# Performance work log

Measured on AMD Instinct MI355X. Metric: run time of the kernel, lower is better.

## Reference

```python
import jax, jax.numpy as jnp
import numpy as np

N_STEPS = 8  # DGL GatedGraphConv n_steps as hardcoded in GatedGCN.__init__


def _gru(a, h, Wih, Whh, bih, bhh):
    # torch.nn.GRUCell: gate order (r, z, n)
    gi = a @ Wih.T + bih          # [N, 3d]
    gh = h @ Whh.T + bhh          # [N, 3d]
    ir, iz, inn = jnp.split(gi, 3, axis=-1)
    hr, hz, hn = jnp.split(gh, 3, axis=-1)
    r = jax.nn.sigmoid(ir + hr)
    z = jax.nn.sigmoid(iz + hz)
    n = jnp.tanh(inn + r * hn)
    return (1.0 - z) * n + z * h


def _gated_conv(h, src, dst, W, b, Wih, Whh, bih, bhh):
    # DGL GatedGraphConv with a single etype: for each step,
    # message = Linear(h[src]); aggregate = sum over in-edges; h = GRU(agg, h)
    N = h.shape[0]

    def step(h, _):
        m = h @ W.T + b                                   # [N, d] linear per node (message fn)
        agg = jax.ops.segment_sum(m[src], dst, num_segments=N)  # [N, d] sum over in-edges
        return _gru(agg, h, Wih, Whh, bih, bhh), None

    h, _ = jax.lax.scan(step, h, None, length=N_STEPS)
    return h


def setup_inputs() -> dict:
    key = jax.random.key(0)
    ks = jax.random.split(key, 10)
    N, E, D = 50000, 800000, 128  # in_feats = h_feats = num_classes = 128
    s = 1.0 / np.sqrt(D)
    return {
        "in_feat": jax.random.normal(ks[0], (N, D), jnp.float32),
        "src": jax.random.randint(ks[1], (E,), 0, N),
        "dst": jax.random.randint(ks[2], (E,), 0, N),
        "W1": jax.random.normal(ks[3], (D, D), jnp.float32) * s,
        "b1": jnp.zeros((D,), jnp.float32),
        "Wih1": jax.random.normal(ks[4], (3 * D, D), jnp.float32) * s,
        "Whh1": jax.random.normal(ks[5], (3 * D, D), jnp.float32) * s,
        "bih1": jnp.zeros((3 * D,), jnp.float32),
        "bhh1": jnp.zeros((3 * D,), jnp.float32),
        "W2": jax.random.normal(ks[6], (D, D), jnp.float32) * s,
        "b2": jnp.zeros((D,), jnp.float32),
        "Wih2": jax.random.normal(ks[7], (3 * D, D), jnp.float32) * s,
        "Whh2": jax.random.normal(ks[8], (3 * D, D), jnp.float32) * s,
        "bih2": jnp.zeros((3 * D,), jnp.float32),
        "bhh2": jnp.zeros((3 * D,), jnp.float32),
    }


def reference(in_feat, src, dst, W1, b1, Wih1, Whh1, bih1, bhh1,
              W2, b2, Wih2, Whh2, bih2, bhh2):
    # in_feats == h_feats so DGL's zero-padding of the input is a no-op here.
    h = _gated_conv(in_feat, src, dst, W1, b1, Wih1, Whh1, bih1, bhh1)
    h = jax.nn.relu(h)
    h = _gated_conv(h, src, dst, W2, b2, Wih2, Whh2, bih2, bhh2)
    # dgl.mean_nodes with a single graph -> [1, num_classes]
    return jnp.mean(h, axis=0, keepdims=True)
```

## Files before the change

kernel.cpp:

```cpp
#include <hip/hip_runtime.h>
#include <hip/hip_bf16.h>
#include <cmath>

#define DD 128

typedef __attribute__((ext_vector_type(8))) short short8v;
typedef __attribute__((ext_vector_type(4))) short short4v;
typedef __attribute__((ext_vector_type(4))) float floatx4;

__device__ __forceinline__ float sigmoid_f(float x) { return 1.0f / (1.0f + __expf(-x)); }
__device__ __forceinline__ float tanh_f(float x) {
  float e = __expf(2.0f * x);
  return 1.0f - 2.0f / (e + 1.0f);
}
__device__ __forceinline__ unsigned short f2bf(float x) {
  __hip_bfloat16 b = __float2bfloat16(x);
  return *reinterpret_cast<unsigned short*>(&b);
}
__device__ __forceinline__ float bf2f(unsigned short s) {
  return __uint_as_float(((unsigned int)s) << 16);
}

__global__ __launch_bounds__(256) void deg_count(const int* __restrict__ dst,
                                                 int* __restrict__ deg, int E) {
  int e = blockIdx.x * blockDim.x + threadIdx.x;
  if (e < E) atomicAdd(&deg[dst[e]], 1);
}

__global__ __launch_bounds__(256) void scan_part(const int* __restrict__ deg,
                                                 int* __restrict__ bsum, int N) {
  __shared__ int s[256];
  int tid = threadIdx.x;
  int i = blockIdx.x * 256 + tid;
  s[tid] = (i < N) ? deg[i] : 0;
  __syncthreads();
  for (int st = 128; st > 0; st >>= 1) {
    if (tid < st) s[tid] += s[tid + st];
    __syncthreads();
  }
  if (tid == 0) bsum[blockIdx.x] = s[0];
}

__global__ __launch_bounds__(256) void scan_top(const int* __restrict__ bsum,
                                                int* __restrict__ bofs, int nb) {
  __shared__ int s[256];
  int tid = threadIdx.x;
  int v = (tid < nb) ? bsum[tid] : 0;
  s[tid] = v;
  __syncthreads();
  for (int o = 1; o < 256; o <<= 1) {
    int t = (tid >= o) ? s[tid - o] : 0;
    __syncthreads();
    s[tid] += t;
    __syncthreads();
  }
  if (tid < nb) bofs[tid] = s[tid] - v;
  if (tid == nb - 1) bofs[nb] = s[tid];
}

__global__ __launch_bounds__(256) void scan_final(const int* __restrict__ deg,
                                                  const int* __restrict__ bofs,
                                                  int* __restrict__ ofs,
                                                  int* __restrict__ cur, int N) {
  __shared__ int s[256];
  int tid = threadIdx.x;
  int i = blockIdx.x * 256 + tid;
  int v = (i < N) ? deg[i] : 0;
  s[tid] = v;
  __syncthreads();
  for (int o = 1; o < 256; o <<= 1) {
    int t = (tid >= o) ? s[tid - o] : 0;
    __syncthreads();
    s[tid] += t;
    __syncthreads();
  }
  int off = bofs[blockIdx.x] + s[tid] - v;
  if (i < N) {
    ofs[i] = off;
    cur[i] = off;
    if (i == N - 1) ofs[N] = off + v;
  }
}

__global__ __launch_bounds__(256) void fill_csr(const int* __restrict__ src,
                                                const int* __restrict__ dst,
                                                int* __restrict__ cur,
                                                int* __restrict__ eidx, int E) {
  int e = blockIdx.x * blockDim.x + threadIdx.x;
  if (e < E) {
    int p = atomicAdd(&cur[dst[e]], 1);
    eidx[p] = src[e];
  }
}

__global__ __launch_bounds__(128) void fuse_w(const float* __restrict__ Wih,
                                              const float* __restrict__ W,
                                              float* __restrict__ Wc32) {
  int r = blockIdx.x;
  int k = threadIdx.x;
  float acc = 0.0f;
  for (int j = 0; j < DD; ++j) acc = fmaf(Wih[r * DD + j], W[j * DD + k], acc);
  Wc32[(size_t)r * DD + k] = acc;
}

__global__ __launch_bounds__(128) void fuse_u(const float* __restrict__ Wih,
                                              const float* __restrict__ b,
                                              float* __restrict__ u) {
  int r = blockIdx.x * 128 + threadIdx.x;
  if (r < 3 * DD) {
    float acc = 0.0f;
    for (int j = 0; j < DD; ++j) acc = fmaf(Wih[r * DD + j], b[j], acc);
    u[r] = acc;
  }
}

__global__ __launch_bounds__(256) void split_w(const float* __restrict__ Wf,
                                               const float* __restrict__ Whh,
                                               unsigned short* __restrict__ Wp) {
  int i = blockIdx.x * 256 + threadIdx.x;
  const int TOT = 6 * DD * DD;
  if (i < TOT) {
    int r = i >> 7;
    float x = (r < 3 * DD) ? Wf[i] : Whh[i - 3 * DD * DD];
    unsigned short hb = f2bf(x);
    float xr = x - bf2f(hb);
    unsigned short mb = f2bf(xr);
    Wp[i] = hb;
    Wp[TOT + i] = mb;
  }
}

__global__ __launch_bounds__(256) void gather_h(const float* __restrict__ h,
                                                const int* __restrict__ ofs,
                                                const int* __restrict__ eidx,
                                                unsigned short* __restrict__ aggp, int N) {
  int node = blockIdx.x * 8 + (threadIdx.x >> 5);
  if (node >= N) return;
  int l = (threadIdx.x & 31) << 2;
  int beg = ofs[node], end = ofs[node + 1];
  float4 aa[4];
#pragma unroll
  for (int j = 0; j < 4; ++j) aa[j] = (float4){0.f, 0.f, 0.f, 0.f};
  int e = beg;
  for (; e + 7 < end; e += 8) {
    float4 v[8];
#pragma unroll
    for (int j = 0; j < 8; ++j)
      v[j] = *(const float4*)(h + (size_t)eidx[e + j] * DD + l);
#pragma unroll
    for (int j = 0; j < 8; ++j) {
      aa[j & 3].x += v[j].x; aa[j & 3].y += v[j].y;
      aa[j & 3].z += v[j].z; aa[j & 3].w += v[j].w;
    }
  }
  for (; e + 1 < end; e += 2) {
    float4 v0 = *(const float4*)(h + (size_t)eidx[e] * DD + l);
    float4 v1 = *(const float4*)(h + (size_t)eidx[e + 1] * DD + l);
    aa[0].x += v0.x; aa[0].y += v0.y; aa[0].z += v0.z; aa[0].w += v0.w;
    aa[1].x += v1.x; aa[1].y += v1.y; aa[1].z += v1.z; aa[1].w += v1.w;
  }
  if (e < end) {
    float4 v = *(const float4*)(h + (size_t)eidx[e] * DD + l);
    aa[0].x += v.x; aa[0].y += v.y; aa[0].z += v.z; aa[0].w += v.w;
  }
  float f[4];
  f[0] = (aa[0].x + aa[1].x) + (aa[2].x + aa[3].x);
  f[1] = (aa[0].y + aa[1].y) + (aa[2].y + aa[3].y);
  f[2] = (aa[0].z + aa[1].z) + (aa[2].z + aa[3].z);
  f[3] = (aa[0].w + aa[1].w) + (aa[2].w + aa[3].w);
  short4v q0, q1;
#pragma unroll
  for (int j = 0; j < 4; ++j) {
    unsigned short hb = f2bf(f[j]);
    float xr = f[j] - bf2f(hb);
    q0[j] = (short)hb;
    q1[j] = (short)f2bf(xr);
  }
  unsigned short* p = aggp + (size_t)node * 256 + l;
  *(short4v*)(p) = q0;
  *(short4v*)(p + 128) = q1;
}

__device__ __forceinline__ void split8_2v(float4 v0, float4 v1, short8v& q0, short8v& q1) {
  float f[8] = {v0.x, v0.y, v0.z, v0.w, v1.x, v1.y, v1.z, v1.w};
#pragma unroll
  for (int e = 0; e < 8; ++e) {
    float x = f[e];
    unsigned short hb = f2bf(x);
    float xr = x - bf2f(hb);
    q0[e] = (short)hb;
    q1[e] = (short)f2bf(xr);
  }
}

__global__ __launch_bounds__(256, 3) void gru_mfma3(
    const unsigned short* __restrict__ Aggp,
    const float* __restrict__ H,
    const unsigned short* __restrict__ Wp,
    const float* __restrict__ bih, const float* __restrict__ bhh,
    const float* __restrict__ u, const int* __restrict__ deg,
    float* __restrict__ Hout, int N, int do_relu)
{
  __shared__ short sB[2][96 * DD];
  const int TOT = 6 * DD * DD;
  const int tid = threadIdx.x;
  const int wid = tid >> 6;
  const int lane = tid & 63;
  const int lrow = lane & 15;
  const int hi = lane >> 4;
  const int lk = hi * 8;
  const int rowBase = blockIdx.x * 128 + wid * 32;
  const int j0 = blockIdx.y * 32;

  floatx4 acc[6][2][2];
#pragma unroll
  for (int g = 0; g < 6; ++g)
#pragma unroll
    for (int ct = 0; ct < 2; ++ct)
#pragma unroll
      for (int rt = 0; rt < 2; ++rt) acc[g][ct][rt] = (floatx4){0.f, 0.f, 0.f, 0.f};

  int r0 = rowBase + lrow;       if (r0 >= N) r0 = N - 1;
  int r1 = rowBase + 16 + lrow;  if (r1 >= N) r1 = N - 1;

  int s_row[6], s_cnk[6];
  size_t s_grow[6];
#pragma unroll
  for (int i = 0; i < 6; ++i) {
    int ch = tid + i * 256;
    s_row[i] = ch >> 4;
    s_cnk[i] = ch & 15;
    s_grow[i] = (size_t)((s_row[i] >> 5) * DD + j0 + (s_row[i] & 31));
  }

#pragma unroll
  for (int arr = 0; arr < 2; ++arr) {
    const size_t gbase = (size_t)arr * 384 * DD;
    if (arr > 0) __syncthreads();

    {
      short8v w0[6], w1[6];
#pragma unroll
      for (int i = 0; i < 6; ++i) {
        w0[i] = *(const short8v*)(Wp + 0 * TOT + gbase + s_grow[i] * DD + s_cnk[i] * 8);
        w1[i] = *(const short8v*)(Wp + 1 * TOT + gbase + s_grow[i] * DD + s_cnk[i] * 8);
      }
#pragma unroll
      for (int i = 0; i < 6; ++i) {
        int off = s_row[i] * DD + (s_cnk[i] ^ (s_row[i] & 7)) * 8;
        *(short8v*)(&sB[0][off]) = w0[i];
        *(short8v*)(&sB[1][off]) = w1[i];
      }
    }
    __syncthreads();

    if (arr == 0) {
      const unsigned short* P0 = Aggp + (size_t)r0 * 256 + lk;
      const unsigned short* P1 = Aggp + (size_t)r1 * 256 + lk;
      __builtin_amdgcn_s_setprio(1);
#pragma unroll
      for (int kc = 0; kc < 4; ++kc) {
        short8v f00 = *(const short8v*)(P0 + kc * 32);
        short8v f10 = *(const short8v*)(P0 + 128 + kc * 32);
        short8v f01 = *(const short8v*)(P1 + kc * 32);
        short8v f11 = *(const short8v*)(P1 + 128 + kc * 32);
#pragma unroll
        for (int gl = 0; gl < 3; ++gl) {
#pragma unroll
          for (int ct = 0; ct < 2; ++ct) {
            int lr = gl * 32 + ct * 16 + lrow;
            int off = lr * DD + ((kc * 4 + hi) ^ (lr & 7)) * 8;
            short8v bh = *(const short8v*)(&sB[0][off]);
            acc[gl][ct][0] = __builtin_amdgcn_mfma_f32_16x16x32_bf16(f00, bh, acc[gl][ct][0], 0, 0, 0);
            acc[gl][ct][0] = __builtin_amdgcn_mfma_f32_16x16x32_bf16(f10, bh, acc[gl][ct][0], 0, 0, 0);
            acc[gl][ct][1] = __builtin_amdgcn_mfma_f32_16x16x32_bf16(f01, bh, acc[gl][ct][1], 0, 0, 0);
            acc[gl][ct][1] = __builtin_amdgcn_mfma_f32_16x16x32_bf16(f11, bh, acc[gl][ct][1], 0, 0, 0);
            short8v bm = *(const short8v*)(&sB[1][off]);
            acc[gl][ct][0] = __builtin_amdgcn_mfma_f32_16x16x32_bf16(f00, bm, acc[gl][ct][0], 0, 0, 0);
            acc[gl][ct][1] = __builtin_amdgcn_mfma_f32_16x16x32_bf16(f01, bm, acc[gl][ct][1], 0, 0, 0);
          }
        }
      }
      __builtin_amdgcn_s_setprio(0);
    } else {
      const float* A0 = H + (size_t)r0 * DD + lk;
      const float* A1 = H + (size_t)r1 * DD + lk;
      float4 pa0 = *(const float4*)(A0);
      float4 pa1 = *(const float4*)(A0 + 4);
      float4 pb0 = *(const float4*)(A1);
      float4 pb1 = *(const float4*)(A1 + 4);

      __builtin_amdgcn_s_setprio(1);
#pragma unroll
      for (int kc = 0; kc < 4; ++kc) {
        float4 qa0, qa1, qb0, qb1;
        if (kc < 3) {
          qa0 = *(const float4*)(A0 + (kc + 1) * 32);
          qa1 = *(const float4*)(A0 + (kc + 1) * 32 + 4);
          qb0 = *(const float4*)(A1 + (kc + 1) * 32);
          qb1 = *(const float4*)(A1 + (kc + 1) * 32 + 4);
        }
        short8v f00, f10, f01, f11;
        split8_2v(pa0, pa1, f00, f10);
        split8_2v(pb0, pb1, f01, f11);
#pragma unroll
        for (int gl = 0; gl < 3; ++gl) {
#pragma unroll
          for (int ct = 0; ct < 2; ++ct) {
            int lr = gl * 32 + ct * 16 + lrow;
            int off = lr * DD + ((kc * 4 + hi) ^ (lr & 7)) * 8;
            short8v bh = *(const short8v*)(&sB[0][off]);
            acc[3 + gl][ct][0] = __builtin_amdgcn_mfma_f32_16x16x32_bf16(f00, bh, acc[3 + gl][ct][0], 0, 0, 0);
            acc[3 + gl][ct][0] = __builtin_amdgcn_mfma_f32_16x16x32_bf16(f10, bh, acc[3 + gl][ct][0], 0, 0, 0);
            acc[3 + gl][ct][1] = __builtin_amdgcn_mfma_f32_16x16x32_bf16(f01, bh, acc[3 + gl][ct][1], 0, 0, 0);
            acc[3 + gl][ct][1] = __builtin_amdgcn_mfma_f32_16x16x32_bf16(f11, bh, acc[3 + gl][ct][1], 0, 0, 0);
            short8v bm = *(const short8v*)(&sB[1][off]);
            acc[3 + gl][ct][0] = __builtin_amdgcn_mfma_f32_16x16x32_bf16(f00, bm, acc[3 + gl][ct][0], 0, 0, 0);
            acc[3 + gl][ct][1] = __builtin_amdgcn_mfma_f32_16x16x32_bf16(f01, bm, acc[3 + gl][ct][1], 0, 0, 0);
          }
        }
        if (kc < 3) { pa0 = qa0; pa1 = qa1; pb0 = qb0; pb1 = qb1; }
      }
      __builtin_amdgcn_s_setprio(0);
    }
  }

  float bi_r[2], bi_z[2], bi_n[2], bh_r[2], bh_z[2], bh_n[2], u_r[2], u_z[2], u_n[2];
#pragma unroll
  for (int ct = 0; ct < 2; ++ct) {
    int c = j0 + ct * 16 + lrow;
    bi_r[ct] = bih[c];  bi_z[ct] = bih[DD + c];  bi_n[ct] = bih[2 * DD + c];
    bh_r[ct] = bhh[c];  bh_z[ct] = bhh[DD + c];  bh_n[ct] = bhh[2 * DD + c];
    u_r[ct]  = u[c];    u_z[ct]  = u[DD + c];    u_n[ct]  = u[2 * DD + c];
  }

#pragma unroll
  for (int rt = 0; rt < 2; ++rt) {
#pragma unroll
    for (int q = 0; q < 4; ++q) {
      int row = rowBase + rt * 16 + hi * 4 + q;
      if (row < N) {
        float dg = (float)deg[row];
#pragma unroll
        for (int ct = 0; ct < 2; ++ct) {
          int c = j0 + ct * 16 + lrow;
          float ir = acc[0][ct][rt][q] + bi_r[ct] + dg * u_r[ct];
          float iz = acc[1][ct][rt][q] + bi_z[ct] + dg * u_z[ct];
          float in = acc[2][ct][rt][q] + bi_n[ct] + dg * u_n[ct];
          float hr = acc[3][ct][rt][q] + bh_r[ct];
          float hz = acc[4][ct][rt][q] + bh_z[ct];
          float hn = acc[5][ct][rt][q] + bh_n[ct];
          float rg = sigmoid_f(ir + hr);
          float zg = sigmoid_f(iz + hz);
          float ng = tanh_f(in + rg * hn);
          float hold = H[(size_t)row * DD + c];
          float out = (1.0f - zg) * ng + zg * hold;
          if (do_relu) out = fmaxf(out, 0.0f);
          Hout[(size_t)row * DD + c] = out;
        }
      }
    }
  }
}

__global__ __launch_bounds__(256) void col_mean(
    const float* __restrict__ H, float* __restrict__ out, int N)
{
  __shared__ float s[256];
  int c = threadIdx.x & 127;
  int rg = threadIdx.x >> 7;
  float acc = 0.0f;
  for (int r = blockIdx.x * 2 + rg; r < N; r += gridDim.x * 2)
    acc += H[(size_t)r * DD + c];
  s[threadIdx.x] = acc;
  __syncthreads();
  if (threadIdx.x < 128) {
    float v = (s[threadIdx.x] + s[threadIdx.x + 128]) * (1.0f / (float)N);
    unsafeAtomicAdd(out + c, v);
  }
}

extern "C" void kernel_launch(void* const* d_in, const int* in_sizes, int n_in,
                              void* d_out, int out_size, void* d_ws, size_t ws_size,
                              hipStream_t stream) {
  const float* in_feat = (const float*)d_in[0];
  const int* src = (const int*)d_in[1];
  const int* dst = (const int*)d_in[2];
  const float* W[2]   = {(const float*)d_in[3], (const float*)d_in[9]};
  const float* bb[2]  = {(const float*)d_in[4], (const float*)d_in[10]};
  const float* Wih[2] = {(const float*)d_in[5], (const float*)d_in[11]};
  const float* Whh[2] = {(const float*)d_in[6], (const float*)d_in[12]};
  const float* bih[2] = {(const float*)d_in[7], (const float*)d_in[13]};
  const float* bhh[2] = {(const float*)d_in[8], (const float*)d_in[14]};
  const int N = in_sizes[0] / DD;
  const int E = in_sizes[1];

  const size_t nd = (size_t)N * DD;
  char* base = (char*)d_ws;
  float* hA  = (float*)base; base += nd * sizeof(float);
  float* hB  = (float*)base; base += nd * sizeof(float);
  unsigned short* aggp = (unsigned short*)base; base += (size_t)N * 256 * sizeof(unsigned short);
  float* Wc32 = (float*)base; base += (size_t)3 * DD * DD * sizeof(float);
  unsigned short* Wp[2];
  Wp[0] = (unsigned short*)base; base += (size_t)2 * 6 * DD * DD * sizeof(unsigned short);
  Wp[1] = (unsigned short*)base; base += (size_t)2 * 6 * DD * DD * sizeof(unsigned short);
  float* u[2];
  u[0] = (float*)base; base += 3 * DD * sizeof(float);
  u[1] = (float*)base; base += 3 * DD * sizeof(float);
  int* deg  = (int*)base; base += (size_t)N * sizeof(int);
  int* ofs  = (int*)base; base += ((size_t)N + 1) * sizeof(int);
  int* cur  = (int*)base; base += (size_t)N * sizeof(int);
  int* eidx = (int*)base; base += (size_t)E * sizeof(int);
  int* bsum = (int*)base; base += 256 * sizeof(int);
  int* bofs = (int*)base; base += 257 * sizeof(int);

  const int nb = (N + 255) / 256;

  hipMemsetAsync(deg, 0, (size_t)N * sizeof(int), stream);
  deg_count<<<(E + 255) / 256, 256, 0, stream>>>(dst, deg, E);
  scan_part<<<nb, 256, 0, stream>>>(deg, bsum, N);
  scan_top<<<1, 256, 0, stream>>>(bsum, bofs, nb);
  scan_final<<<nb, 256, 0, stream>>>(deg, bofs, ofs, cur, N);
  fill_csr<<<(E + 255) / 256, 256, 0, stream>>>(src, dst, cur, eidx, E);

  for (int layer = 0; layer < 2; ++layer) {
    fuse_w<<<3 * DD, 128, 0, stream>>>(Wih[layer], W[layer], Wc32);
    split_w<<<(6 * DD * DD + 255) / 256, 256, 0, stream>>>(Wc32, Whh[layer], Wp[layer]);
    fuse_u<<<3, 128, 0, stream>>>(Wih[layer], bb[layer], u[layer]);
  }

  hipMemcpyAsync(hA, in_feat, nd * sizeof(float), hipMemcpyDeviceToDevice, stream);

  float* hcur = hA;
  float* hnxt = hB;
  const int gblocks = (N + 7) / 8;
  const int mblocks = (N + 127) / 128;

  for (int layer = 0; layer < 2; ++layer) {
    for (int step_i = 0; step_i < 8; ++step_i) {
      gather_h<<<gblocks, 256, 0, stream>>>(hcur, ofs, eidx, aggp, N);
      int do_relu = (layer == 0 && step_i == 7) ? 1 : 0;
      gru_mfma3<<<dim3(mblocks, 4), 256, 0, stream>>>(
          aggp, hcur, Wp[layer], bih[layer], bhh[layer],
          u[layer], deg, hnxt, N, do_relu);
      float* t = hcur; hcur = hnxt; hnxt = t;
    }
  }

  hipMemsetAsync(d_out, 0, DD * sizeof(float), stream);
  col_mean<<<256, 256, 0, stream>>>(hcur, (float*)d_out, N);
}
```

Baseline: 1.813 ms.

## Halve GRU tile rows and single-buffer weight LDS to raise occupancy

The GRU MFMA kernel now gives each wave 16 rows instead of 32 (64 rows per block), roughly doubling the grid. Only one half of the split bf16 weight slab sits in shared memory at a time, loaded in two passes with extra barriers. A-fragments are preloaded before the weight passes, and launch bounds rise to 4 blocks per CU. This cuts LDS and register footprint to raise occupancy, but each block reloads the full weights from global/L2 for half as many rows and synchronises more often.

```diff
diff --git a/kernel.cpp b/kernel.cpp
--- a/kernel.cpp
+++ b/kernel.cpp
@@ -193,7 +193,7 @@
   }
 }
 
-__global__ __launch_bounds__(256, 3) void gru_mfma3(
+__global__ __launch_bounds__(256, 4) void gru_mfma3(
     const unsigned short* __restrict__ Aggp,
     const float* __restrict__ H,
     const unsigned short* __restrict__ Wp,
@@ -201,7 +201,7 @@
     const float* __restrict__ u, const int* __restrict__ deg,
     float* __restrict__ Hout, int N, int do_relu)
 {
-  __shared__ short sB[2][96 * DD];
+  __shared__ short sB[96 * DD];
   const int TOT = 6 * DD * DD;
   const int tid = threadIdx.x;
   const int wid = tid >> 6;
@@ -209,19 +209,17 @@
   const int lrow = lane & 15;
   const int hi = lane >> 4;
   const int lk = hi * 8;
-  const int rowBase = blockIdx.x * 128 + wid * 32;
+  const int rowBase = blockIdx.x * 64 + wid * 16;
   const int j0 = blockIdx.y * 32;
 
-  floatx4 acc[6][2][2];
+  floatx4 acc[6][2];
 #pragma unroll
   for (int g = 0; g < 6; ++g)
 #pragma unroll
-    for (int ct = 0; ct < 2; ++ct)
-#pragma unroll
-      for (int rt = 0; rt < 2; ++rt) acc[g][ct][rt] = (floatx4){0.f, 0.f, 0.f, 0.f};
-
-  int r0 = rowBase + lrow;       if (r0 >= N) r0 = N - 1;
-  int r1 = rowBase + 16 + lrow;  if (r1 >= N) r1 = N - 1;
+    for (int ct = 0; ct < 2; ++ct) acc[g][ct] = (floatx4){0.f, 0.f, 0.f, 0.f};
+
+  int r0 = rowBase + lrow;
+  if (r0 >= N) r0 = N - 1;
 
   int s_row[6], s_cnk[6];
   size_t s_grow[6];
@@ -236,90 +234,57 @@
 #pragma unroll
   for (int arr = 0; arr < 2; ++arr) {
     const size_t gbase = (size_t)arr * 384 * DD;
-    if (arr > 0) __syncthreads();
-
-    {
-      short8v w0[6], w1[6];
-#pragma unroll
-      for (int i = 0; i < 6; ++i) {
-        w0[i] = *(const short8v*)(Wp + 0 * TOT + gbase + s_grow[i] * DD + s_cnk[i] * 8);
-        w1[i] = *(const short8v*)(Wp + 1 * TOT + gbase + s_grow[i] * DD + s_cnk[i] * 8);
+
+    short8v frag0[4], frag1[4];
+    if (arr == 0) {
+      const unsigned short* P0 = Aggp + (size_t)r0 * 256 + lk;
+#pragma unroll
+      for (int kc = 0; kc < 4; ++kc) {
+        frag0[kc] = *(const short8v*)(P0 + kc * 32);
+        frag1[kc] = *(const short8v*)(P0 + 128 + kc * 32);
       }
-#pragma unroll
-      for (int i = 0; i < 6; ++i) {
-        int off = s_row[i] * DD + (s_cnk[i] ^ (s_row[i] & 7)) * 8;
-        *(short8v*)(&sB[0][off]) = w0[i];
-        *(short8v*)(&sB[1][off]) = w1[i];
+    } else {
+      const float* A0 = H + (size_t)r0 * DD + lk;
+#pragma unroll
+      for (int kc = 0; kc < 4; ++kc) {
+        float4 v0 = *(const float4*)(A0 + kc * 32);
+        float4 v1 = *(const float4*)(A0 + kc * 32 + 4);
+        split8_2v(v0, v1, frag0[kc], frag1[kc]);
       }
     }
-    __syncthreads();
-
-    if (arr == 0) {
-      const unsigned short* P0 = Aggp + (size_t)r0 * 256 + lk;
-      const unsigned short* P1 = Aggp + (size_t)r1 * 256 + lk;
+
+#pragma unroll
+    for (int wp = 0; wp < 2; ++wp) {
+      if (arr > 0 || wp > 0) __syncthreads();
+      {
+        short8v w[6];
+#pragma unroll
+        for (int i = 0; i < 6; ++i)
+          w[i] = *(const short8v*)(Wp + (size_t)wp * TOT + gbase + s_grow[i] * DD + s_cnk[i] * 8);
+#pragma unroll
+        for (int i = 0; i < 6; ++i) {
+          int off = s_row[i] * DD + (s_cnk[i] ^ (s_row[i] & 7)) * 8;
+          *(short8v*)(&sB[off]) = w[i];
+        }
+      }
+      __syncthreads();
+
       __builtin_amdgcn_s_setprio(1);
 #pragma unroll
       for (int kc = 0; kc < 4; ++kc) {
-        short8v f00 = *(const short8v*)(P0 + kc * 32);
-        short8v f10 = *(const short8v*)(P0 + 128 + kc * 32);
-        short8v f01 = *(const short8v*)(P1 + kc * 32);
-        short8v f11 = *(const short8v*)(P1 + 128 + kc * 32);
 #pragma unroll
         for (int gl = 0; gl < 3; ++gl) {
 #pragma unroll
           for (int ct = 0; ct < 2; ++ct) {
             int lr = gl * 32 + ct * 16 + lrow;
             int off = lr * DD + ((kc * 4 + hi) ^ (lr & 7)) * 8;
-            short8v bh = *(const short8v*)(&sB[0][off]);
-            acc[gl][ct][0] = __builtin_amdgcn_mfma_f32_16x16x32_bf16(f00, bh, acc[gl][ct][0], 0, 0, 0);
-            acc[gl][ct][0] = __builtin_amdgcn_mfma_f32_16x16x32_bf16(f10, bh, acc[gl][ct][0], 0, 0, 0);
-            acc[gl][ct][1] = __builtin_amdgcn_mfma_f32_16x16x32_bf16(f01, bh, acc[gl][ct][1], 0, 0, 0);
-            acc[gl][ct][1] = __builtin_amdgcn_mfma_f32_16x16x32_bf16(f11, bh, acc[gl][ct][1], 0, 0, 0);
-            short8v bm = *(const short8v*)(&sB[1][off]);
-            acc[gl][ct][0] = __builtin_amdgcn_mfma_f32_16x16x32_bf16(f00, bm, acc[gl][ct][0], 0, 0, 0);
-            acc[gl][ct][1] = __builtin_amdgcn_mfma_f32_16x16x32_bf16(f01, bm, acc[gl][ct][1], 0, 0, 0);
+            short8v b = *(const short8v*)(&sB[off]);
+            const int g = arr * 3 + gl;
+            acc[g][ct] = __builtin_amdgcn_mfma_f32_16x16x32_bf16(frag0[kc], b, acc[g][ct], 0, 0, 0);
+            if (wp == 0)
+              acc[g][ct] = __builtin_amdgcn_mfma_f32_16x16x32_bf16(frag1[kc], b, acc[g][ct], 0, 0, 0);
           }
         }
-      }
-      __builtin_amdgcn_s_setprio(0);
-    } else {
-      const float* A0 = H + (size_t)r0 * DD + lk;
-      const float* A1 = H + (size_t)r1 * DD + lk;
-      float4 pa0 = *(const float4*)(A0);
-      float4 pa1 = *(const float4*)(A0 + 4);
-      float4 pb0 = *(const float4*)(A1);
-      float4 pb1 = *(const float4*)(A1 + 4);
-
-      __builtin_amdgcn_s_setprio(1);
-#pragma unroll
-      for (int kc = 0; kc < 4; ++kc) {
-        float4 qa0, qa1, qb0, qb1;
-        if (kc < 3) {
-          qa0 = *(const float4*)(A0 + (kc + 1) * 32);
-          qa1 = *(const float4*)(A0 + (kc + 1) * 32 + 4);
-          qb0 = *(const float4*)(A1 + (kc + 1) * 32);
-          qb1 = *(const float4*)(A1 + (kc + 1) * 32 + 4);
-        }
-        short8v f00, f10, f01, f11;
-        split8_2v(pa0, pa1, f00, f10);
-        split8_2v(pb0, pb1, f01, f11);
-#pragma unroll
-        for (int gl = 0; gl < 3; ++gl) {
-#pragma unroll
-          for (int ct = 0; ct < 2; ++ct) {
-            int lr = gl * 32 + ct * 16 + lrow;
-            int off = lr * DD + ((kc * 4 + hi) ^ (lr & 7)) * 8;
-            short8v bh = *(const short8v*)(&sB[0][off]);
-            acc[3 + gl][ct][0] = __builtin_amdgcn_mfma_f32_16x16x32_bf16(f00, bh, acc[3 + gl][ct][0], 0, 0, 0);
-            acc[3 + gl][ct][0] = __builtin_amdgcn_mfma_f32_16x16x32_bf16(f10, bh, acc[3 + gl][ct][0], 0, 0, 0);
-            acc[3 + gl][ct][1] = __builtin_amdgcn_mfma_f32_16x16x32_bf16(f01, bh, acc[3 + gl][ct][1], 0, 0, 0);
-            acc[3 + gl][ct][1] = __builtin_amdgcn_mfma_f32_16x16x32_bf16(f11, bh, acc[3 + gl][ct][1], 0, 0, 0);
-            short8v bm = *(const short8v*)(&sB[1][off]);
-            acc[3 + gl][ct][0] = __builtin_amdgcn_mfma_f32_16x16x32_bf16(f00, bm, acc[3 + gl][ct][0], 0, 0, 0);
-            acc[3 + gl][ct][1] = __builtin_amdgcn_mfma_f32_16x16x32_bf16(f01, bm, acc[3 + gl][ct][1], 0, 0, 0);
-          }
-        }
-        if (kc < 3) { pa0 = qa0; pa1 = qa1; pb0 = qb0; pb1 = qb1; }
       }
       __builtin_amdgcn_s_setprio(0);
     }
@@ -335,29 +300,26 @@
   }
 
 #pragma unroll
-  for (int rt = 0; rt < 2; ++rt) {
-#pragma unroll
-    for (int q = 0; q < 4; ++q) {
-      int row = rowBase + rt * 16 + hi * 4 + q;
-      if (row < N) {
-        float dg = (float)deg[row];
-#pragma unroll
-        for (int ct = 0; ct < 2; ++ct) {
-          int c = j0 + ct * 16 + lrow;
-          float ir = acc[0][ct][rt][q] + bi_r[ct] + dg * u_r[ct];
-          float iz = acc[1][ct][rt][q] + bi_z[ct] + dg * u_z[ct];
-          float in = acc[2][ct][rt][q] + bi_n[ct] + dg * u_n[ct];
-          float hr = acc[3][ct][rt][q] + bh_r[ct];
-          float hz = acc[4][ct][rt][q] + bh_z[ct];
-          float hn = acc[5][ct][rt][q] + bh_n[ct];
-          float rg = sigmoid_f(ir + hr);
-          float zg = sigmoid_f(iz + hz);
-          float ng = tanh_f(in + rg * hn);
-          float hold = H[(size_t)row * DD + c];
-          float out = (1.0f - zg) * ng + zg * hold;
-          if (do_relu) out = fmaxf(out, 0.0f);
-          Hout[(size_t)row * DD + c] = out;
-        }
+  for (int q = 0; q < 4; ++q) {
+    int row = rowBase + hi * 4 + q;
+    if (row < N) {
+      float dg = (float)deg[row];
+#pragma unroll
+      for (int ct = 0; ct < 2; ++ct) {
+        int c = j0 + ct * 16 + lrow;
+        float ir = acc[0][ct][q] + bi_r[ct] + dg * u_r[ct];
+        float iz = acc[1][ct][q] + bi_z[ct] + dg * u_z[ct];
+        float in = acc[2][ct][q] + bi_n[ct] + dg * u_n[ct];
+        float hr = acc[3][ct][q] + bh_r[ct];
+        float hz = acc[4][ct][q] + bh_z[ct];
+        float hn = acc[5][ct][q] + bh_n[ct];
+        float rg = sigmoid_f(ir + hr);
+        float zg = sigmoid_f(iz + hz);
+        float ng = tanh_f(in + rg * hn);
+        float hold = H[(size_t)row * DD + c];
+        float out = (1.0f - zg) * ng + zg * hold;
+        if (do_relu) out = fmaxf(out, 0.0f);
+        Hout[(size_t)row * DD + c] = out;
       }
     }
   }
@@ -434,13 +396,13 @@
   float* hcur = hA;
   float* hnxt = hB;
   const int gblocks = (N + 7) / 8;
-  const int mblocks = (N + 127) / 128;
+  const int mblocks64 = (N + 63) / 64;
 
   for (int layer = 0; layer < 2; ++layer) {
     for (int step_i = 0; step_i < 8; ++step_i) {
       gather_h<<<gblocks, 256, 0, stream>>>(hcur, ofs, eidx, aggp, N);
       int do_relu = (layer == 0 && step_i == 7) ? 1 : 0;
-      gru_mfma3<<<dim3(mblocks, 4), 256, 0, stream>>>(
+      gru_mfma3<<<dim3(mblocks64, 4), 256, 0, stream>>>(
           aggp, hcur, Wp[layer], bih[layer], bhh[layer],
           u[layer], deg, hnxt, N, do_relu);
       float* t = hcur; hcur = hnxt; hnxt = t;
```

Result: no change. 1.844 ms (+1.7%).
